# Kernel optimization log

Hardware: AMD Instinct MI355X
Metric: run time of the kernel (lower is better)

## Reference

```python
import math
import jax, jax.numpy as jnp
import numpy as np

RATIO = 0.1

def setup_inputs() -> dict:
    key = jax.random.key(0)
    ks = jax.random.split(key, 8)
    B, S, D = 8, 4096, 2048
    transformer_out = jax.random.normal(ks[0], (B, S, D), jnp.float32)
    hidden_states = jax.random.normal(ks[1], (B, S, D), jnp.float32)
    lengths = jax.random.randint(ks[2], (B,), S // 2, S + 1)
    attention_mask = (jnp.arange(S)[None, :] < lengths[:, None]).astype(jnp.int32)
    s = 1.0 / math.sqrt(D)
    W1 = jax.random.normal(ks[3], (D, D), jnp.float32) * s
    b1 = jnp.zeros((D,), jnp.float32)
    w2 = jax.random.normal(ks[4], (D,), jnp.float32) * s
    b2 = jnp.zeros((), jnp.float32)
    Wv = jax.random.normal(ks[5], (D, D), jnp.float32) * s
    bv = jnp.zeros((D,), jnp.float32)
    return dict(transformer_out=transformer_out, hidden_states=hidden_states,
                attention_mask=attention_mask, W1=W1, b1=b1, w2=w2, b2=b2, Wv=Wv, bv=bv)

def reference(transformer_out, hidden_states, attention_mask, W1, b1, w2, b2, Wv, bv):
    B, S, D = transformer_out.shape
    M = math.ceil(S * RATIO)  # static upper bound on max_nugget (n_nugget <= ceil(S*ratio))
    # scorer MLP: Linear(D,D) -> ReLU -> Linear(D,1), squeezed
    h = jax.nn.relu(jnp.einsum('bsd,de->bse', transformer_out, W1) + b1)
    scores = jnp.einsum('bse,e->bs', h, w2) + b2                      # [B,S]
    maskb = attention_mask.astype(bool)
    scores = jnp.where(maskb, scores, jnp.finfo(scores.dtype).min)    # masked fill
    n_token = maskb.sum(axis=1)                                        # [B]
    n_nugget = jnp.ceil(n_token.astype(scores.dtype) * RATIO).astype(jnp.int32)
    n_nugget = jnp.minimum(jnp.maximum(n_nugget, 1), n_token)
    nugget_mask = jnp.arange(M)[None, :] < n_nugget[:, None]          # [B,M] ragged validity
    # descending top-k by double argsort, then stable reorder to original token order
    sorted_idx = jnp.argsort(-scores, axis=1)[:, :M]                   # [B,M]
    big = jnp.iinfo(sorted_idx.dtype).max
    resort = jnp.where(nugget_mask, sorted_idx, big)
    indices = jnp.take_along_axis(sorted_idx, jnp.argsort(resort, axis=1), axis=1)
    enc = jnp.take_along_axis(hidden_states, indices[:, :, None], axis=1)  # [B,M,D]
    enc = jnp.einsum('bmd,de->bme', enc, Wv) + bv                      # value_ffn
    nugget_scores = jnp.take_along_axis(scores, indices, axis=1)       # [B,M]
    return enc, nugget_mask, nugget_scores, indices, scores
```

## Files before the change

### kernel.cpp

```cpp
#include <hip/hip_runtime.h>
#include <float.h>
#include <math.h>

typedef _Float16 h16;
typedef _Float16 h16x8 __attribute__((ext_vector_type(8)));
typedef float    f32x4 __attribute__((ext_vector_type(4)));

#define MFMA16(a, b, c) __builtin_amdgcn_mfma_f32_16x16x32_f16((a), (b), (c), 0, 0, 0)

#define B_    8
#define S_    4096
#define D_    2048
#define M_    410
#define MROWS (B_ * S_)
#define R2    (B_ * M_)

#define MASK_FILL (-3.3895313892515355e38f)

#define ENC_OFF  0
#define MASK_OFF (B_ * M_ * D_)
#define NSC_OFF  (MASK_OFF + B_ * M_)
#define IDX_OFF  (NSC_OFF + B_ * M_)
#define SC_OFF   (IDX_OFF + B_ * M_)

#define WS_W1T  ((size_t)0)
#define WS_WVT  ((size_t)8  << 20)
#define WS_PART ((size_t)16 << 20)
#define WS_IDX  ((size_t)17 << 20)
#define WS_NEEDED (((size_t)17 << 20) + R2 * sizeof(int))

__device__ inline float finite_or(float v, float alt) {
    return (v == v && v <= FLT_MAX && v >= -FLT_MAX) ? v : alt;
}

__device__ inline void gload_lds16(const h16* g, h16* l) {
    __builtin_amdgcn_global_load_lds(
        (const __attribute__((address_space(1))) void*)g,
        (__attribute__((address_space(3))) void*)l, 16, 0, 0);
}

__device__ inline h16x8 cvt8(f32x4 a, f32x4 b) {
    h16x8 r;
#pragma unroll
    for (int i = 0; i < 4; ++i) { r[i] = (h16)a[i]; r[i + 4] = (h16)b[i]; }
    return r;
}

__global__ __launch_bounds__(256) void transpose_kernel(
    const float* __restrict__ W1, const float* __restrict__ Wv,
    h16* __restrict__ w1t, h16* __restrict__ wvt)
{
    __shared__ float tile[32][33];
    const float* src = blockIdx.z ? Wv : W1;
    h16* dt = blockIdx.z ? wvt : w1t;
    const int tx = threadIdx.x, ty = threadIdx.y;
    const int n0 = blockIdx.x * 32, k0 = blockIdx.y * 32;
#pragma unroll
    for (int i = 0; i < 4; ++i) {
        int k = k0 + ty + i * 8;
        tile[ty + i * 8][tx] = src[(size_t)k * D_ + n0 + tx];
    }
    __syncthreads();
#pragma unroll
    for (int i = 0; i < 4; ++i) {
        int n = n0 + ty + i * 8;
        dt[(size_t)n * D_ + k0 + tx] = (h16)tile[tx][ty + i * 8];
    }
}

#define PH_SYNC do { __builtin_amdgcn_s_barrier(); \
    asm volatile("s_waitcnt lgkmcnt(0)" ::: "memory"); \
    __builtin_amdgcn_sched_barrier(0); } while (0)
#define PH_END  __builtin_amdgcn_s_barrier()

#define QUAD(mb, nb2) do { \
    __builtin_amdgcn_s_setprio(1); \
    _Pragma("unroll") for (int i_ = 0; i_ < 4; ++i_) \
    _Pragma("unroll") for (int jn_ = 0; jn_ < 2; ++jn_) \
    _Pragma("unroll") for (int ks_ = 0; ks_ < 2; ++ks_) \
        acc[(mb) + i_][(nb2) + jn_] = \
            MFMA16(fa[ks_][i_], fb[ks_][jn_], acc[(mb) + i_][(nb2) + jn_]); \
    __builtin_amdgcn_s_setprio(0); } while (0)

__global__ __launch_bounds__(512, 2) void gemm8_kernel(
    const float* __restrict__ A,
    const h16* __restrict__ Bt,
    const float* __restrict__ bias,
    const float* __restrict__ w2,
    float* __restrict__ outp)
{
    constexpr int NT = 32;
    __shared__ h16 As[2][256][64];
    __shared__ h16 Bs[2][256][64];
    __shared__ float red[4][256];

    const int pn = blockIdx.y & 7;
    const int pm = blockIdx.x + 8 * (blockIdx.y >> 3);
    const int t = threadIdx.x;
    const int lane = t & 63, wid = t >> 6;
    const int wm = wid >> 2, wn = wid & 3;
    const int l15 = lane & 15, kseg = lane >> 4;
    const int pc0 = kseg ^ (l15 & 7);

    const int sc = (t & 7) ^ ((t >> 3) & 7);
    const float* Ag = A  + (size_t)(pm * 256 + (t >> 3)) * D_ + sc * 8;
    const h16*   Bg = Bt + (size_t)(pn * 256 + (t >> 3)) * D_ + sc * 8;
    char* AsB = (char*)&As[0][0][0];
    char* BsB = (char*)&Bs[0][0][0];

    f32x4 ar[8];
    f32x4 acc[8][4] = {};
    h16x8 fa[2][4], fb[2][2];

    auto A_issue = [&](int kt) {
#pragma unroll
        for (int j = 0; j < 4; ++j) {
            const float* p = Ag + (size_t)j * 64 * D_ + kt * 64;
            ar[2 * j]     = *(const f32x4*)p;
            ar[2 * j + 1] = *(const f32x4*)(p + 4);
        }
    };
    auto B_issue = [&](int kt, int nb) {
#pragma unroll
        for (int j = 0; j < 4; ++j)
            gload_lds16(Bg + (size_t)j * 64 * D_ + kt * 64,
                        (h16*)(BsB + nb * 65536 + j * 8192 + wid * 1024));
    };
    auto A_write = [&](int nb) {
#pragma unroll
        for (int j = 0; j < 4; ++j)
            *(h16x8*)(AsB + nb * 65536 + j * 8192 + t * 16) =
                cvt8(ar[2 * j], ar[2 * j + 1]);
    };
    auto LDA = [&](int cb, int mb) {
#pragma unroll
        for (int i = 0; i < 4; ++i) {
            const int row = wm * 128 + (mb + i) * 16 + l15;
#pragma unroll
            for (int ks = 0; ks < 2; ++ks)
                fa[ks][i] = *(const h16x8*)&As[cb][row][(pc0 ^ (ks << 2)) * 8];
        }
    };
    auto LDB = [&](int cb, int nb2) {
#pragma unroll
        for (int i = 0; i < 2; ++i) {
            const int row = wn * 64 + (nb2 + i) * 16 + l15;
#pragma unroll
            for (int ks = 0; ks < 2; ++ks)
                fb[ks][i] = *(const h16x8*)&Bs[cb][row][(pc0 ^ (ks << 2)) * 8];
        }
    };

    A_issue(0);
    B_issue(0, 0);
    A_write(0);
    asm volatile("s_waitcnt vmcnt(0) lgkmcnt(0)" ::: "memory");
    __builtin_amdgcn_s_barrier();

    for (int kt = 0; kt < NT; ++kt) {
        const int cb = kt & 1;
        const bool more = (kt + 1 < NT);
        LDA(cb, 0); LDB(cb, 0);
        if (more) { A_issue(kt + 1); B_issue(kt + 1, cb ^ 1); }
        PH_SYNC; QUAD(0, 0); PH_END;
        LDB(cb, 2);
        PH_SYNC; QUAD(0, 2); PH_END;
        LDA(cb, 4);
        PH_SYNC; QUAD(4, 2); PH_END;
        LDB(cb, 0);
        if (more) A_write(cb ^ 1);
        PH_SYNC; QUAD(4, 0);
        asm volatile("s_waitcnt vmcnt(0) lgkmcnt(0)" ::: "memory");
        PH_END;
    }
    __syncthreads();

    float vout[8][4];
#pragma unroll
    for (int fm = 0; fm < 8; ++fm)
#pragma unroll
        for (int rg = 0; rg < 4; ++rg) vout[fm][rg] = 0.0f;
#pragma unroll
    for (int fn = 0; fn < 4; ++fn) {
        int ng = pn * 256 + wn * 64 + fn * 16 + l15;
        float w = w2[ng], bb = bias[ng];
#pragma unroll
        for (int fm = 0; fm < 8; ++fm)
#pragma unroll
            for (int rg = 0; rg < 4; ++rg) {
                float c = acc[fm][fn][rg] + bb;
                c = fmaxf(c, 0.0f);
                vout[fm][rg] += c * w;
            }
    }
#pragma unroll
    for (int off = 1; off < 16; off <<= 1)
#pragma unroll
        for (int fm = 0; fm < 8; ++fm)
#pragma unroll
            for (int rg = 0; rg < 4; ++rg)
                vout[fm][rg] += __shfl_xor(vout[fm][rg], off);
    if (l15 == 0) {
#pragma unroll
        for (int fm = 0; fm < 8; ++fm)
#pragma unroll
            for (int rg = 0; rg < 4; ++rg)
                red[wn][wm * 128 + fm * 16 + kseg * 4 + rg] = vout[fm][rg];
    }
    __syncthreads();
    if (t < 256) {
        float s = red[0][t] + red[1][t] + red[2][t] + red[3][t];
        outp[(size_t)pn * MROWS + pm * 256 + t] = s;
    }
}

template <int MODE>
__global__ __launch_bounds__(512, 4) void gemm_kernel(
    const float* __restrict__ A, const h16* __restrict__ Bt,
    const float* __restrict__ bias, const float* __restrict__ w2,
    float* __restrict__ outp, const int* __restrict__ gidx)
{
    constexpr int BM = 128, BN = 256, BK = 32;
    constexpr int NT = D_ / BK;
    __shared__ h16 As[3][BM][32];
    __shared__ h16 Bs[3][BN][32];
    __shared__ float red[4][128];

    const int pn = blockIdx.x, pm = blockIdx.y;
    const int t = threadIdx.x;
    const int lane = t & 63, wid = t >> 6;
    const int wm = wid >> 2, wn = wid & 3;
    const int l15 = lane & 15, kseg = lane >> 4;
    const int pcf = (kseg ^ ((l15 >> 1) & 3)) * 8;

    const int arow = t >> 2, aseg = t & 3;
    const int pcA = (aseg ^ ((arow >> 1) & 3)) * 8;
    const int lrow   = lane >> 2;
    const int lchunk = (lane & 3) ^ ((lane >> 3) & 3);

    const float* Ap;
    if constexpr (MODE == 0) {
        Ap = A + (size_t)(pm * BM + arow) * D_ + aseg * 8;
    } else {
        int r = pm * BM + arow;
        int rr = (r < R2) ? r : R2 - 1;
        int bb = rr / M_;
        int tok = gidx[rr];
        Ap = A + ((size_t)bb * S_ + tok) * D_ + aseg * 8;
    }
    const h16* gB0 = Bt + (size_t)(pn * BN + 32 * wid + lrow)      * D_ + lchunk * 8;
    const h16* gB1 = Bt + (size_t)(pn * BN + 32 * wid + 16 + lrow) * D_ + lchunk * 8;

    f32x4 acc[4][4] = {};

    f32x4 a0 = *(const f32x4*)Ap, a1 = *(const f32x4*)(Ap + 4);
    *(h16x8*)&As[0][arow][pcA] = cvt8(a0, a1);
    gload_lds16(gB0, &Bs[0][32 * wid][0]);
    gload_lds16(gB1, &Bs[0][32 * wid + 16][0]);
    gB0 += BK; gB1 += BK;
    Ap += BK;
    a0 = *(const f32x4*)Ap; a1 = *(const f32x4*)(Ap + 4);
    gload_lds16(gB0, &Bs[1][32 * wid][0]);
    gload_lds16(gB1, &Bs[1][32 * wid + 16][0]);
    gB0 += BK; gB1 += BK;
    asm volatile("s_waitcnt vmcnt(0) lgkmcnt(0)" ::: "memory");
    __builtin_amdgcn_s_barrier();

    for (int kt = 0; kt < NT; ++kt) {
        const int cb = kt % 3;
        if (kt > 0) {
            if (kt + 1 < NT) {
                asm volatile("s_waitcnt vmcnt(4) lgkmcnt(0)" ::: "memory");
            } else {
                asm volatile("s_waitcnt vmcnt(0) lgkmcnt(0)" ::: "memory");
            }
            __builtin_amdgcn_s_barrier();
        }
        if (kt + 1 < NT) {
            *(h16x8*)&As[(kt + 1) % 3][arow][pcA] = cvt8(a0, a1);
            if (kt + 2 < NT) {
                Ap += BK;
                a0 = *(const f32x4*)Ap; a1 = *(const f32x4*)(Ap + 4);
                const int nb = (kt + 2) % 3;
                gload_lds16(gB0, &Bs[nb][32 * wid][0]);
                gload_lds16(gB1, &Bs[nb][32 * wid + 16][0]);
                gB0 += BK; gB1 += BK;
            }
        }
        h16x8 fa[4];
#pragma unroll
        for (int fm = 0; fm < 4; ++fm) {
            int row = wm * 64 + fm * 16 + l15;
            fa[fm] = *(const h16x8*)&As[cb][row][pcf];
        }
#pragma unroll
        for (int fn = 0; fn < 4; ++fn) {
            int row = wn * 64 + fn * 16 + l15;
            h16x8 fb = *(const h16x8*)&Bs[cb][row][pcf];
#pragma unroll
            for (int fm = 0; fm < 4; ++fm)
                acc[fm][fn] = MFMA16(fa[fm], fb, acc[fm][fn]);
        }
    }
    __syncthreads();

    if constexpr (MODE == 0) {
    } else {
#pragma unroll
        for (int fn = 0; fn < 4; ++fn) {
            int ng = pn * BN + wn * 64 + fn * 16 + l15;
            float bb = bias[ng];
#pragma unroll
            for (int fm = 0; fm < 4; ++fm) {
                int rbase = pm * BM + wm * 64 + fm * 16 + kseg * 4;
#pragma unroll
                for (int rg = 0; rg < 4; ++rg) {
                    int r = rbase + rg;
                    if (r < R2)
                        outp[(size_t)r * D_ + ng] =
                            finite_or(acc[fm][fn][rg] + bb, 0.0f);
                }
            }
        }
    }
}

__global__ __launch_bounds__(256) void score_reduce_kernel(
    const float* __restrict__ part, const float* __restrict__ b2,
    const int* __restrict__ amask, float* __restrict__ outF)
{
    int m = blockIdx.x * 256 + threadIdx.x;
    float v = b2[0];
#pragma unroll
    for (int p = 0; p < 8; ++p) v += part[(size_t)p * MROWS + m];
    v = finite_or(v, 0.0f);
    if (amask[m] == 0) v = MASK_FILL;
    outF[SC_OFF + m] = v;
}

__global__ __launch_bounds__(1024) void topk_kernel(
    const float* __restrict__ scores, const int* __restrict__ amask,
    float* __restrict__ outF, int* __restrict__ idx_ws)
{
    const int b = blockIdx.x, t = threadIdx.x;
    __shared__ float s[S_];
    __shared__ int perm[S_];
    __shared__ int sel[512];
    __shared__ int wsum[16];

    int cnt = 0;
    for (int i = t; i < S_; i += 1024) {
        float v = scores[b * S_ + i];
        s[i] = v; perm[i] = i;
        cnt += amask[b * S_ + i];
    }
#pragma unroll
    for (int off = 1; off < 64; off <<= 1) cnt += __shfl_xor(cnt, off);
    if ((t & 63) == 0) wsum[t >> 6] = cnt;
    __syncthreads();
    int n_token = 0;
#pragma unroll
    for (int w = 0; w < 16; ++w) n_token += wsum[w];
    int nn = (int)ceilf((float)n_token * 0.1f);
    if (nn < 1) nn = 1;
    if (nn > n_token) nn = n_token;

    for (int k = 2; k <= S_; k <<= 1)
        for (int j = k >> 1; j > 0; j >>= 1) {
            __syncthreads();
            for (int i = t; i < S_; i += 1024) {
                int ixj = i ^ j;
                if (ixj > i) {
                    int a = perm[i], c = perm[ixj];
                    bool ok = (s[a] > s[c]) || (s[a] == s[c] && a < c);
                    if (((i & k) == 0) ? !ok : ok) { perm[i] = c; perm[ixj] = a; }
                }
            }
        }
    __syncthreads();
    for (int i = t; i < 512; i += 1024) sel[i] = (i < nn) ? perm[i] : 0x7fffffff;
    for (int k = 2; k <= 512; k <<= 1)
        for (int j = k >> 1; j > 0; j >>= 1) {
            __syncthreads();
            if (t < 512) {
                int i = t, ixj = i ^ j;
                if (ixj > i) {
                    int a = sel[i], c = sel[ixj];
                    if (((i & k) == 0) ? (a > c) : (a < c)) { sel[i] = c; sel[ixj] = a; }
                }
            }
        }
    __syncthreads();
    for (int m = t; m < M_; m += 1024) {
        int idx = (m < nn) ? sel[m] : perm[m];
        outF[MASK_OFF + b * M_ + m] = (m < nn) ? 1.0f : 0.0f;
        outF[NSC_OFF + b * M_ + m]  = s[idx];
        outF[IDX_OFF + b * M_ + m]  = (float)idx;
        idx_ws[b * M_ + m] = idx;
    }
}

extern "C" void kernel_launch(void* const* d_in, const int* in_sizes, int n_in,
                              void* d_out, int out_size, void* d_ws, size_t ws_size,
                              hipStream_t stream)
{
    const float* T  = (const float*)d_in[0];
    const float* H  = (const float*)d_in[1];
    const int*   AM = (const int*)d_in[2];
    const float* W1 = (const float*)d_in[3];
    const float* b1 = (const float*)d_in[4];
    const float* w2 = (const float*)d_in[5];
    const float* b2 = (const float*)d_in[6];
    const float* Wv = (const float*)d_in[7];
    const float* bv = (const float*)d_in[8];
    float* outF = (float*)d_out;
    char* ws = (char*)d_ws;

    if (ws_size < WS_NEEDED) return;

    h16* w1t  = (h16*)(ws + WS_W1T);
    h16* wvt  = (h16*)(ws + WS_WVT);
    float* part = (float*)(ws + WS_PART);
    int* idxw   = (int*)(ws + WS_IDX);

    transpose_kernel<<<dim3(64, 64, 2), dim3(32, 8), 0, stream>>>(
        W1, Wv, w1t, wvt);
    gemm8_kernel<<<dim3(8, 128), 512, 0, stream>>>(
        T, w1t, b1, w2, part);
    score_reduce_kernel<<<dim3(128), 256, 0, stream>>>(part, b2, AM, outF);
    topk_kernel<<<dim3(8), 1024, 0, stream>>>(outF + SC_OFF, AM, outF, idxw);
    gemm_kernel<1><<<dim3(8, 26), 512, 0, stream>>>(
        H, wvt, bv, nullptr, outF + ENC_OFF, idxw);
}
```

Measured before the change: 563.6 us.

## Pre-convert activations to fp16 and stage both GEMM operands via direct LDS loads

Adds a pass that converts the fp32 transformer output to fp16 in workspace, so the large scorer GEMM can load both A and B tiles with global_load_lds straight into shared memory instead of loading fp32 through registers, converting, and writing. This cuts register pressure and VALU work inside the main loop but adds a full extra read and write pass over the 256MB activation tensor. A fallback path using the generic gemm_kernel with a new fused ReLU/w2 epilogue is added for small workspaces. The value GEMM also drops from triple to double buffering with simpler barriers.

```diff
diff --git a/kernel.cpp b/kernel.cpp
--- a/kernel.cpp
+++ b/kernel.cpp
@@ -27,7 +27,9 @@
 #define WS_WVT  ((size_t)8  << 20)
 #define WS_PART ((size_t)16 << 20)
 #define WS_IDX  ((size_t)17 << 20)
-#define WS_NEEDED (((size_t)17 << 20) + R2 * sizeof(int))
+#define WS_A16  ((size_t)18 << 20)
+#define WS_NEED_SMALL (((size_t)17 << 20) + R2 * sizeof(int))
+#define WS_NEED_BIG   (WS_A16 + (size_t)MROWS * D_ * sizeof(h16))
 
 __device__ inline float finite_or(float v, float alt) {
     return (v == v && v <= FLT_MAX && v >= -FLT_MAX) ? v : alt;
@@ -44,6 +46,18 @@
 #pragma unroll
     for (int i = 0; i < 4; ++i) { r[i] = (h16)a[i]; r[i + 4] = (h16)b[i]; }
     return r;
+}
+
+__global__ __launch_bounds__(256) void precvt_kernel(
+    const float* __restrict__ T, h16* __restrict__ A16)
+{
+    const size_t n = (size_t)MROWS * D_;
+    for (size_t i = ((size_t)blockIdx.x * 256 + threadIdx.x) * 8; i < n;
+         i += (size_t)gridDim.x * 256 * 8) {
+        f32x4 a = *(const f32x4*)(T + i);
+        f32x4 b = *(const f32x4*)(T + i + 4);
+        *(h16x8*)(A16 + i) = cvt8(a, b);
+    }
 }
 
 __global__ __launch_bounds__(256) void transpose_kernel(
@@ -82,8 +96,8 @@
             MFMA16(fa[ks_][i_], fb[ks_][jn_], acc[(mb) + i_][(nb2) + jn_]); \
     __builtin_amdgcn_s_setprio(0); } while (0)
 
-__global__ __launch_bounds__(512, 2) void gemm8_kernel(
-    const float* __restrict__ A,
+__global__ __launch_bounds__(512, 2) void gemm8v2_kernel(
+    const h16* __restrict__ A16,
     const h16* __restrict__ Bt,
     const float* __restrict__ bias,
     const float* __restrict__ w2,
@@ -103,35 +117,24 @@
     const int pc0 = kseg ^ (l15 & 7);
 
     const int sc = (t & 7) ^ ((t >> 3) & 7);
-    const float* Ag = A  + (size_t)(pm * 256 + (t >> 3)) * D_ + sc * 8;
-    const h16*   Bg = Bt + (size_t)(pn * 256 + (t >> 3)) * D_ + sc * 8;
+    const h16* Ag = A16 + (size_t)(pm * 256 + (t >> 3)) * D_ + sc * 8;
+    const h16* Bg = Bt  + (size_t)(pn * 256 + (t >> 3)) * D_ + sc * 8;
     char* AsB = (char*)&As[0][0][0];
     char* BsB = (char*)&Bs[0][0][0];
 
-    f32x4 ar[8];
     f32x4 acc[8][4] = {};
     h16x8 fa[2][4], fb[2][2];
 
-    auto A_issue = [&](int kt) {
-#pragma unroll
-        for (int j = 0; j < 4; ++j) {
-            const float* p = Ag + (size_t)j * 64 * D_ + kt * 64;
-            ar[2 * j]     = *(const f32x4*)p;
-            ar[2 * j + 1] = *(const f32x4*)(p + 4);
-        }
-    };
-    auto B_issue = [&](int kt, int nb) {
+    auto STAGE = [&](int kt, int nb) {
+#pragma unroll
+        for (int j = 0; j < 4; ++j)
+            gload_lds16(Ag + (size_t)j * 64 * D_ + kt * 64,
+                        (h16*)(AsB + nb * 65536 + j * 8192 + wid * 1024));
 #pragma unroll
         for (int j = 0; j < 4; ++j)
             gload_lds16(Bg + (size_t)j * 64 * D_ + kt * 64,
                         (h16*)(BsB + nb * 65536 + j * 8192 + wid * 1024));
     };
-    auto A_write = [&](int nb) {
-#pragma unroll
-        for (int j = 0; j < 4; ++j)
-            *(h16x8*)(AsB + nb * 65536 + j * 8192 + t * 16) =
-                cvt8(ar[2 * j], ar[2 * j + 1]);
-    };
     auto LDA = [&](int cb, int mb) {
 #pragma unroll
         for (int i = 0; i < 4; ++i) {
@@ -151,26 +154,22 @@
         }
     };
 
-    A_issue(0);
-    B_issue(0, 0);
-    A_write(0);
-    asm volatile("s_waitcnt vmcnt(0) lgkmcnt(0)" ::: "memory");
+    STAGE(0, 0);
+    asm volatile("s_waitcnt vmcnt(0)" ::: "memory");
     __builtin_amdgcn_s_barrier();
 
     for (int kt = 0; kt < NT; ++kt) {
         const int cb = kt & 1;
-        const bool more = (kt + 1 < NT);
         LDA(cb, 0); LDB(cb, 0);
-        if (more) { A_issue(kt + 1); B_issue(kt + 1, cb ^ 1); }
+        if (kt + 1 < NT) STAGE(kt + 1, cb ^ 1);
         PH_SYNC; QUAD(0, 0); PH_END;
         LDB(cb, 2);
         PH_SYNC; QUAD(0, 2); PH_END;
         LDA(cb, 4);
         PH_SYNC; QUAD(4, 2); PH_END;
         LDB(cb, 0);
-        if (more) A_write(cb ^ 1);
         PH_SYNC; QUAD(4, 0);
-        asm volatile("s_waitcnt vmcnt(0) lgkmcnt(0)" ::: "memory");
+        asm volatile("s_waitcnt vmcnt(0)" ::: "memory");
         PH_END;
     }
     __syncthreads();
@@ -222,11 +221,17 @@
 {
     constexpr int BM = 128, BN = 256, BK = 32;
     constexpr int NT = D_ / BK;
-    __shared__ h16 As[3][BM][32];
-    __shared__ h16 Bs[3][BN][32];
+    __shared__ h16 As[2][BM][32];
+    __shared__ h16 Bs[2][BN][32];
     __shared__ float red[4][128];
 
-    const int pn = blockIdx.x, pm = blockIdx.y;
+    int pn, pm;
+    if constexpr (MODE == 0) {
+        pn = blockIdx.y & 7;
+        pm = blockIdx.x + 8 * (blockIdx.y >> 3);
+    } else {
+        pn = blockIdx.x; pm = blockIdx.y;
+    }
     const int t = threadIdx.x;
     const int lane = t & 63, wid = t >> 6;
     const int wm = wid >> 2, wn = wid & 3;
@@ -260,51 +265,71 @@
     gB0 += BK; gB1 += BK;
     Ap += BK;
     a0 = *(const f32x4*)Ap; a1 = *(const f32x4*)(Ap + 4);
-    gload_lds16(gB0, &Bs[1][32 * wid][0]);
-    gload_lds16(gB1, &Bs[1][32 * wid + 16][0]);
-    gB0 += BK; gB1 += BK;
-    asm volatile("s_waitcnt vmcnt(0) lgkmcnt(0)" ::: "memory");
-    __builtin_amdgcn_s_barrier();
+    __syncthreads();
 
     for (int kt = 0; kt < NT; ++kt) {
-        const int cb = kt % 3;
-        if (kt > 0) {
-            if (kt + 1 < NT) {
-                asm volatile("s_waitcnt vmcnt(4) lgkmcnt(0)" ::: "memory");
-            } else {
-                asm volatile("s_waitcnt vmcnt(0) lgkmcnt(0)" ::: "memory");
-            }
-            __builtin_amdgcn_s_barrier();
-        }
+        const int cur = kt & 1;
         if (kt + 1 < NT) {
-            *(h16x8*)&As[(kt + 1) % 3][arow][pcA] = cvt8(a0, a1);
-            if (kt + 2 < NT) {
-                Ap += BK;
-                a0 = *(const f32x4*)Ap; a1 = *(const f32x4*)(Ap + 4);
-                const int nb = (kt + 2) % 3;
-                gload_lds16(gB0, &Bs[nb][32 * wid][0]);
-                gload_lds16(gB1, &Bs[nb][32 * wid + 16][0]);
-                gB0 += BK; gB1 += BK;
-            }
+            *(h16x8*)&As[cur ^ 1][arow][pcA] = cvt8(a0, a1);
+            gload_lds16(gB0, &Bs[cur ^ 1][32 * wid][0]);
+            gload_lds16(gB1, &Bs[cur ^ 1][32 * wid + 16][0]);
+            gB0 += BK; gB1 += BK;
+        }
+        if (kt + 2 < NT) {
+            Ap += BK;
+            a0 = *(const f32x4*)Ap; a1 = *(const f32x4*)(Ap + 4);
         }
         h16x8 fa[4];
 #pragma unroll
         for (int fm = 0; fm < 4; ++fm) {
             int row = wm * 64 + fm * 16 + l15;
-            fa[fm] = *(const h16x8*)&As[cb][row][pcf];
+            fa[fm] = *(const h16x8*)&As[cur][row][pcf];
         }
 #pragma unroll
         for (int fn = 0; fn < 4; ++fn) {
             int row = wn * 64 + fn * 16 + l15;
-            h16x8 fb = *(const h16x8*)&Bs[cb][row][pcf];
+            h16x8 fb = *(const h16x8*)&Bs[cur][row][pcf];
 #pragma unroll
             for (int fm = 0; fm < 4; ++fm)
                 acc[fm][fn] = MFMA16(fa[fm], fb, acc[fm][fn]);
         }
-    }
-    __syncthreads();
+        __syncthreads();
+    }
 
     if constexpr (MODE == 0) {
+        float vout[4][4] = {};
+#pragma unroll
+        for (int fn = 0; fn < 4; ++fn) {
+            int ng = pn * BN + wn * 64 + fn * 16 + l15;
+            float w = w2[ng], bb = bias[ng];
+#pragma unroll
+            for (int fm = 0; fm < 4; ++fm)
+#pragma unroll
+                for (int rg = 0; rg < 4; ++rg) {
+                    float c = acc[fm][fn][rg] + bb;
+                    c = fmaxf(c, 0.0f);
+                    vout[fm][rg] += c * w;
+                }
+        }
+#pragma unroll
+        for (int off = 1; off < 16; off <<= 1)
+#pragma unroll
+            for (int fm = 0; fm < 4; ++fm)
+#pragma unroll
+                for (int rg = 0; rg < 4; ++rg)
+                    vout[fm][rg] += __shfl_xor(vout[fm][rg], off);
+        if (l15 == 0) {
+#pragma unroll
+            for (int fm = 0; fm < 4; ++fm)
+#pragma unroll
+                for (int rg = 0; rg < 4; ++rg)
+                    red[wn][wm * 64 + fm * 16 + kseg * 4 + rg] = vout[fm][rg];
+        }
+        __syncthreads();
+        if (t < 128) {
+            float s = red[0][t] + red[1][t] + red[2][t] + red[3][t];
+            outp[(size_t)pn * MROWS + pm * BM + t] = s;
+        }
     } else {
 #pragma unroll
         for (int fn = 0; fn < 4; ++fn) {
@@ -416,7 +441,7 @@
     float* outF = (float*)d_out;
     char* ws = (char*)d_ws;
 
-    if (ws_size < WS_NEEDED) return;
+    if (ws_size < WS_NEED_SMALL) return;
 
     h16* w1t  = (h16*)(ws + WS_W1T);
     h16* wvt  = (h16*)(ws + WS_WVT);
@@ -425,8 +450,16 @@
 
     transpose_kernel<<<dim3(64, 64, 2), dim3(32, 8), 0, stream>>>(
         W1, Wv, w1t, wvt);
-    gemm8_kernel<<<dim3(8, 128), 512, 0, stream>>>(
-        T, w1t, b1, w2, part);
+
+    if (ws_size >= WS_NEED_BIG) {
+        h16* a16 = (h16*)(ws + WS_A16);
+        precvt_kernel<<<dim3(2048), 256, 0, stream>>>(T, a16);
+        gemm8v2_kernel<<<dim3(8, 128), 512, 0, stream>>>(
+            a16, w1t, b1, w2, part);
+    } else {
+        gemm_kernel<0><<<dim3(8, 256), 512, 0, stream>>>(
+            T, w1t, b1, w2, part, nullptr);
+    }
     score_reduce_kernel<<<dim3(128), 256, 0, stream>>>(part, b2, AM, outF);
     topk_kernel<<<dim3(8), 1024, 0, stream>>>(outF + SC_OFF, AM, outF, idxw);
     gemm_kernel<1><<<dim3(8, 26), 512, 0, stream>>>(
```

Result: faster. 536.1 us (-4.9%).
